# Kernel optimization log

Measured on AMD Instinct MI355X. Metric: run time of the kernel, lower is better.

## Reference

```python
import jax, jax.numpy as jnp
import numpy as np

L = 12; NH = 12; DH = 64; H = 768; FF = 3072; S = 1024; B = 4; V = 50265; WIN = 256  # one-sided window (attention_window=512)

def _ln(x, g, b, eps=1e-5):
    m = jnp.mean(x, axis=-1, keepdims=True)
    v = jnp.mean((x - m) ** 2, axis=-1, keepdims=True)
    return (x - m) * jax.lax.rsqrt(v + eps) * g + b

def _local_attn(q, k, v, mask, w):
    # q,k,v: [B,NH,S,DH]; mask: [B,S] ints (1=attend, 0=pad).
    # Sliding-window attention computed in query blocks of size w over key spans of 3w
    # (no global tokens: forward never passes a global_attention_mask).
    b, nh, s, dh = q.shape
    c = w; nb = s // c; span = 3 * c
    qb = q.reshape(b, nh, nb, c, dh)
    kp = jnp.pad(k, ((0, 0), (0, 0), (w, w), (0, 0)))
    vp = jnp.pad(v, ((0, 0), (0, 0), (w, w), (0, 0)))
    idx = jnp.arange(nb)[:, None] * c + jnp.arange(span)[None, :]  # [nb, span]
    kb = kp[:, :, idx]  # [B,NH,nb,span,DH]
    vb = vp[:, :, idx]
    scores = jnp.einsum('bhncd,bhnkd->bhnck', qb, kb) / np.float32(np.sqrt(dh))
    qi = jnp.arange(c)[:, None]; kj = jnp.arange(span)[None, :]
    band = (kj - qi >= 0) & (kj - qi <= 2 * w)  # |k_abs - q_abs| <= w
    mp = jnp.pad(mask, ((0, 0), (w, w)))  # zero pad also masks out-of-range keys
    mb = mp[:, idx] > 0  # [B, nb, span]
    ok = band[None, None, None, :, :] & mb[:, None, :, None, :]
    scores = jnp.where(ok, scores, jnp.float32(-1e9))
    probs = jax.nn.softmax(scores, axis=-1)
    out = jnp.einsum('bhnck,bhnkd->bhncd', probs, vb)
    return out.reshape(b, nh, s, dh)

def _forward(WE, PE, Eg, Eb, Wq, bq, Wk, bk, Wv, bv, Wo, bo, g1, beta1, W1, b1, W2, b2, g2, beta2, aw, Wc, bc, input_ids, attention_mask):
    b, s = input_ids.shape
    h = WE[input_ids] + PE[jnp.arange(s)]
    h = _ln(h, Eg, Eb)
    for l in range(L):
        q = (h @ Wq[l] + bq[l]).reshape(b, s, NH, DH).transpose(0, 2, 1, 3)
        k = (h @ Wk[l] + bk[l]).reshape(b, s, NH, DH).transpose(0, 2, 1, 3)
        v = (h @ Wv[l] + bv[l]).reshape(b, s, NH, DH).transpose(0, 2, 1, 3)
        a = _local_attn(q, k, v, attention_mask, WIN)
        a = a.transpose(0, 2, 1, 3).reshape(b, s, H) @ Wo[l] + bo[l]
        h = _ln(h + a, g1[l], beta1[l])
        f = jax.nn.gelu(h @ W1[l] + b1[l], approximate=False) @ W2[l] + b2[l]
        h = _ln(h + f, g2[l], beta2[l])
    # attention-pooling head: softmax over seq of h @ aw, weighted sum, linear classifier
    sc = h @ aw  # [B,S]
    probs = jax.nn.softmax(sc, axis=1)
    pooled = jnp.sum(h * probs[..., None], axis=1)  # [B,H]
    return pooled @ Wc + bc  # [B,1] (dropout is identity in eval)

def setup_inputs():
    key = jax.random.key(0)
    ks = jax.random.split(key, 16)
    n = lambda k, shape: 0.02 * jax.random.normal(k, shape, dtype=jnp.float32)
    return {
        'WE': n(ks[0], (V, H)), 'PE': n(ks[1], (S, H)),
        'Eg': jnp.ones((H,), jnp.float32), 'Eb': jnp.zeros((H,), jnp.float32),
        'Wq': n(ks[2], (L, H, H)), 'bq': jnp.zeros((L, H), jnp.float32),
        'Wk': n(ks[3], (L, H, H)), 'bk': jnp.zeros((L, H), jnp.float32),
        'Wv': n(ks[4], (L, H, H)), 'bv': jnp.zeros((L, H), jnp.float32),
        'Wo': n(ks[5], (L, H, H)), 'bo': jnp.zeros((L, H), jnp.float32),
        'g1': jnp.ones((L, H), jnp.float32), 'beta1': jnp.zeros((L, H), jnp.float32),
        'W1': n(ks[6], (L, H, FF)), 'b1': jnp.zeros((L, FF), jnp.float32),
        'W2': n(ks[7], (L, FF, H)), 'b2': jnp.zeros((L, H), jnp.float32),
        'g2': jnp.ones((L, H), jnp.float32), 'beta2': jnp.zeros((L, H), jnp.float32),
        'aw': jax.random.normal(ks[8], (H,), dtype=jnp.float32),
        'Wc': n(ks[9], (H, 1)), 'bc': jnp.zeros((1,), jnp.float32),
        'input_ids': jax.random.randint(ks[10], (B, S), 0, V, dtype=jnp.int32),
        'attention_mask': jnp.ones((B, S), jnp.int32),
    }

def reference(WE, PE, Eg, Eb, Wq, bq, Wk, bk, Wv, bv, Wo, bo, g1, beta1, W1, b1, W2, b2, g2, beta2, aw, Wc, bc, input_ids, attention_mask):
    return _forward(WE, PE, Eg, Eb, Wq, bq, Wk, bk, Wv, bv, Wo, bo, g1, beta1, W1, b1, W2, b2, g2, beta2, aw, Wc, bc, input_ids, attention_mask)
```

## Files before the change

kernel.cpp:

```cpp
#include <hip/hip_runtime.h>
#include <hip/hip_bf16.h>

#define LAYERS 12
#define NHEAD  12
#define DHEAD  64
#define HDIM   768
#define FFDIM  3072
#define SEQ    1024
#define BATCH  4
#define WINSZ  256
#define MTOK   (BATCH*SEQ)
#define PLANE  ((size_t)MTOK*HDIM)

typedef unsigned short u16;
typedef unsigned int   u32;

using f32x4  = __attribute__((ext_vector_type(4))) float;
using bf16x8 = __attribute__((ext_vector_type(8))) short;

__device__ __forceinline__ float bflo(u32 u){ union{u32 i;float f;}x; x.i = u << 16; return x.f; }
__device__ __forceinline__ float bfhi(u32 u){ union{u32 i;float f;}x; x.i = u & 0xffff0000u; return x.f; }
__device__ __forceinline__ u16 f2bf(float f){
    union{float f;u32 u;}x; x.f = f;
    u32 r = x.u + 0x7fffu + ((x.u >> 16) & 1u);
    return (u16)(r >> 16);
}
__device__ __forceinline__ void gload16(const u16* g, u16* l) {
    __builtin_amdgcn_global_load_lds(
        (const __attribute__((address_space(1))) u32*)g,
        (__attribute__((address_space(3))) u32*)l, 16, 0, 0);
}

__device__ __forceinline__ float wave_sum(float v) {
#pragma unroll
    for (int o = 32; o > 0; o >>= 1) v += __shfl_down(v, o, 64);
    return v;
}
__device__ __forceinline__ float wave_max(float v) {
#pragma unroll
    for (int o = 32; o > 0; o >>= 1) v = fmaxf(v, __shfl_down(v, o, 64));
    return v;
}
__device__ __forceinline__ float blk_sum256(float v, float* sm) {
    v = wave_sum(v);
    int lane = threadIdx.x & 63, w = threadIdx.x >> 6;
    __syncthreads();
    if (lane == 0) sm[w] = v;
    __syncthreads();
    return sm[0] + sm[1] + sm[2] + sm[3];
}
__device__ __forceinline__ float blk_sum1024(float v, float* sm) {
    v = wave_sum(v);
    int lane = threadIdx.x & 63, w = threadIdx.x >> 6;
    __syncthreads();
    if (lane == 0) sm[w] = v;
    __syncthreads();
    float r = 0.f;
#pragma unroll
    for (int i = 0; i < 16; i++) r += sm[i];
    return r;
}
__device__ __forceinline__ float blk_max1024(float v, float* sm) {
    v = wave_max(v);
    int lane = threadIdx.x & 63, w = threadIdx.x >> 6;
    __syncthreads();
    if (lane == 0) sm[w] = v;
    __syncthreads();
    float r = -1e30f;
#pragma unroll
    for (int i = 0; i < 16; i++) r = fmaxf(r, sm[i]);
    return r;
}

__global__ __launch_bounds__(256) void k_embed_ln(
    const float* __restrict__ WE, const float* __restrict__ PE,
    const float* __restrict__ g, const float* __restrict__ bta,
    const int* __restrict__ ids, float* __restrict__ h, u16* __restrict__ hb)
{
    __shared__ float sm[4];
    int tok = blockIdx.x;
    int s = tok & (SEQ - 1);
    int id = ids[tok];
    int tt = threadIdx.x;
    float4 x = make_float4(0.f, 0.f, 0.f, 0.f);
    if (tt < HDIM / 4) {
        float4 a = ((const float4*)(WE + (size_t)id * HDIM))[tt];
        float4 b = ((const float4*)(PE + (size_t)s * HDIM))[tt];
        x = make_float4(a.x + b.x, a.y + b.y, a.z + b.z, a.w + b.w);
    }
    float s1 = blk_sum256(x.x + x.y + x.z + x.w, sm);
    float s2 = blk_sum256(x.x*x.x + x.y*x.y + x.z*x.z + x.w*x.w, sm);
    float mean = s1 * (1.f / HDIM);
    float var  = s2 * (1.f / HDIM) - mean * mean;
    float inv  = rsqrtf(var + 1e-5f);
    if (tt < HDIM / 4) {
        float4 gg = ((const float4*)g)[tt];
        float4 bb = ((const float4*)bta)[tt];
        float4 o;
        o.x = (x.x - mean) * inv * gg.x + bb.x;
        o.y = (x.y - mean) * inv * gg.y + bb.y;
        o.z = (x.z - mean) * inv * gg.z + bb.z;
        o.w = (x.w - mean) * inv * gg.w + bb.w;
        ((float4*)(h + (size_t)tok * HDIM))[tt] = o;
        uint2 pk;
        pk.x = (u32)f2bf(o.x) | ((u32)f2bf(o.y) << 16);
        pk.y = (u32)f2bf(o.z) | ((u32)f2bf(o.w) << 16);
        ((uint2*)(hb + (size_t)tok * HDIM))[tt] = pk;
    }
}

__global__ __launch_bounds__(256) void k_addln(
    float* __restrict__ h, const float* __restrict__ t,
    const float* __restrict__ g, const float* __restrict__ bta, u16* __restrict__ hb)
{
    __shared__ float sm[4];
    int tok = blockIdx.x;
    int tt = threadIdx.x;
    float4 x = make_float4(0.f, 0.f, 0.f, 0.f);
    if (tt < HDIM / 4) {
        float4 a = ((const float4*)(h + (size_t)tok * HDIM))[tt];
        float4 b = ((const float4*)(t + (size_t)tok * HDIM))[tt];
        x = make_float4(a.x + b.x, a.y + b.y, a.z + b.z, a.w + b.w);
    }
    float s1 = blk_sum256(x.x + x.y + x.z + x.w, sm);
    float s2 = blk_sum256(x.x*x.x + x.y*x.y + x.z*x.z + x.w*x.w, sm);
    float mean = s1 * (1.f / HDIM);
    float var  = s2 * (1.f / HDIM) - mean * mean;
    float inv  = rsqrtf(var + 1e-5f);
    if (tt < HDIM / 4) {
        float4 gg = ((const float4*)g)[tt];
        float4 bb = ((const float4*)bta)[tt];
        float4 o;
        o.x = (x.x - mean) * inv * gg.x + bb.x;
        o.y = (x.y - mean) * inv * gg.y + bb.y;
        o.z = (x.z - mean) * inv * gg.z + bb.z;
        o.w = (x.w - mean) * inv * gg.w + bb.w;
        ((float4*)(h + (size_t)tok * HDIM))[tt] = o;
        uint2 pk;
        pk.x = (u32)f2bf(o.x) | ((u32)f2bf(o.y) << 16);
        pk.y = (u32)f2bf(o.z) | ((u32)f2bf(o.w) << 16);
        ((uint2*)(hb + (size_t)tok * HDIM))[tt] = pk;
    }
}

__global__ __launch_bounds__(256) void k_cvtT(
    const float* __restrict__ W, u16* __restrict__ dst, int K, int N,
    size_t ss, size_t ds)
{
    __shared__ float t[32][33];
    W   += (size_t)blockIdx.z * ss;
    dst += (size_t)blockIdx.z * ds;
    int n0 = blockIdx.x * 32, k0 = blockIdx.y * 32;
    int c = threadIdx.x & 31, r8 = threadIdx.x >> 5;
#pragma unroll
    for (int p = 0; p < 4; p++) {
        int k = r8 + p * 8;
        t[k][c] = W[(size_t)(k0 + k) * N + n0 + c];
    }
    __syncthreads();
#pragma unroll
    for (int p = 0; p < 2; p++) {
        int idx = threadIdx.x + p * 256;
        int n = idx >> 4, kp = idx & 15;
        float a = t[kp*2][n], b = t[kp*2+1][n];
        u32 pk = (u32)f2bf(a) | ((u32)f2bf(b) << 16);
        u32* d = (u32*)(dst + (size_t)(n0 + n) * K + k0);
        d[kp] = pk;
    }
}

template<int BM, int BN, int MODE>
__global__ __launch_bounds__(256) void k_gemm_mfma(
    const u16* __restrict__ A, const u16* __restrict__ BT,
    const float* __restrict__ b0, const float* __restrict__ b1, const float* __restrict__ b2,
    void* __restrict__ C, int K, int N)
{
    __shared__ u16 As[2 * BM * 32];
    __shared__ u16 Bs[2 * BN * 32];
    const int tid = threadIdx.x, lane = tid & 63, w = tid >> 6;
    const int bm = blockIdx.y * BM, bn = blockIdx.x * BN;
    constexpr int MT = BM / 32, NT = BN / 32;
    constexpr int AR = BM / 4, BR = BN / 4;
    constexpr int AI = AR / 16, BI = BR / 16;
    const int wm = (w & 1) * (BM / 2), wn = (w >> 1) * (BN / 2);

    f32x4 acc[MT][NT];
#pragma unroll
    for (int mi = 0; mi < MT; mi++)
#pragma unroll
        for (int ni = 0; ni < NT; ni++) acc[mi][ni] = (f32x4){0.f, 0.f, 0.f, 0.f};

    const u16* ag = A  + (size_t)(bm + w * AR + (lane >> 2)) * K + (lane & 3) * 8;
    const u16* bg = BT + (size_t)(bn + w * BR + (lane >> 2)) * K + (lane & 3) * 8;
    u16* al = As + w * AR * 32;
    u16* bl = Bs + w * BR * 32;
    const int fr = lane & 15, fq = (lane >> 4) * 8;

    for (int k0 = 0; k0 < K; k0 += 64) {
#pragma unroll
        for (int s = 0; s < 2; s++) {
#pragma unroll
            for (int i = 0; i < AI; i++)
                gload16(ag + (size_t)i * 16 * K + k0 + s * 32, al + s * BM * 32 + i * 512);
#pragma unroll
            for (int i = 0; i < BI; i++)
                gload16(bg + (size_t)i * 16 * K + k0 + s * 32, bl + s * BN * 32 + i * 512);
        }
        __syncthreads();
#pragma unroll
        for (int s = 0; s < 2; s++) {
            bf16x8 af[MT], bf[NT];
#pragma unroll
            for (int mi = 0; mi < MT; mi++)
                af[mi] = *(const bf16x8*)(As + s * BM * 32 + (wm + mi * 16 + fr) * 32 + fq);
#pragma unroll
            for (int ni = 0; ni < NT; ni++)
                bf[ni] = *(const bf16x8*)(Bs + s * BN * 32 + (wn + ni * 16 + fr) * 32 + fq);
#pragma unroll
            for (int mi = 0; mi < MT; mi++)
#pragma unroll
                for (int ni = 0; ni < NT; ni++)
                    acc[mi][ni] = __builtin_amdgcn_mfma_f32_16x16x32_bf16(af[mi], bf[ni], acc[mi][ni], 0, 0, 0);
        }
        __syncthreads();
    }

#pragma unroll
    for (int mi = 0; mi < MT; mi++) {
        int m_base = bm + wm + mi * 16 + (lane >> 4) * 4;
#pragma unroll
        for (int ni = 0; ni < NT; ni++) {
            int n_g = bn + wn + ni * 16 + (lane & 15);
            const float* bp = b0; int nn = n_g; int which = 0;
            if (MODE == 1) {
                if (n_g >= 1536)      { bp = b2; nn = n_g - 1536; which = 2; }
                else if (n_g >= 768)  { bp = b1; nn = n_g - 768;  which = 1; }
            }
            float bias = bp[nn];
#pragma unroll
            for (int r = 0; r < 4; r++) {
                int m_g = m_base + r;
                float val = acc[mi][ni][r] + bias;
                if (MODE == 0) {
                    ((float*)C)[(size_t)m_g * N + n_g] = val;
                } else if (MODE == 1) {
                    int bb = m_g >> 10, ss = m_g & 1023;
                    int hh = nn >> 6, dd = nn & 63;
                    ((u16*)C)[(size_t)which * PLANE + (((size_t)bb * NHEAD + hh) * SEQ + ss) * DHEAD + dd] = f2bf(val);
                } else {
                    val = 0.5f * val * (1.f + erff(val * 0.70710678118f));
                    ((u16*)C)[(size_t)m_g * N + n_g] = f2bf(val);
                }
            }
        }
    }
}

#define PADW 72
__global__ __launch_bounds__(256) void k_attn_mfma(
    const u16* __restrict__ qkv, const int* __restrict__ mask, u16* __restrict__ abuf)
{
    __shared__ u16 Qs[64 * PADW];
    __shared__ u16 Ks[64 * PADW];
    __shared__ u16 Vt[64 * PADW];
    __shared__ u16 Ps[64 * PADW];
    __shared__ int ms[64];
    const int tid = threadIdx.x, lane = tid & 63, w = tid >> 6;
    int blk = blockIdx.x;
    int qt = blk & 15;
    int hh = (blk >> 4) % NHEAD;
    int b  = blk / (16 * NHEAD);
    int q0 = qt * 64;

    const u16* qp = qkv + ((size_t)b * NHEAD + hh) * SEQ * DHEAD;
    const u16* kp = qp + PLANE;
    const u16* vp = qp + 2 * PLANE;

#pragma unroll
    for (int it = 0; it < 2; it++) {
        int idx = tid + it * 256;
        int r = idx >> 3, c8 = (idx & 7) * 8;
        uint4 u = *(const uint4*)(qp + (size_t)(q0 + r) * DHEAD + c8);
        *(uint4*)(Qs + r * PADW + c8) = u;
    }

    const int fr = lane & 15, g4 = (lane >> 4) * 4, fq = (lane >> 4) * 8;
    const int wq = w * 16;
    const int qpos = q0 + wq + g4;

    f32x4 o[4];
#pragma unroll
    for (int d = 0; d < 4; d++) o[d] = (f32x4){0.f, 0.f, 0.f, 0.f};
    float mr[4], ll[4];
#pragma unroll
    for (int r = 0; r < 4; r++) { mr[r] = -1e9f; ll[r] = 0.f; }

    __syncthreads();
    bf16x8 aq[2];
#pragma unroll
    for (int ks = 0; ks < 2; ks++)
        aq[ks] = *(const bf16x8*)(Qs + (wq + fr) * PADW + ks * 32 + fq);

    for (int ch = 0; ch < 9; ch++) {
        int kbase = q0 - 256 + ch * 64;
        __syncthreads();
#pragma unroll
        for (int it = 0; it < 2; it++) {
            int idx = tid + it * 256;
            int r = idx >> 3, c8 = (idx & 7) * 8;
            int kq = kbase + r;
            uint4 u = (kq >= 0 && kq < SEQ)
                ? *(const uint4*)(kp + (size_t)kq * DHEAD + c8)
                : make_uint4(0u, 0u, 0u, 0u);
            *(uint4*)(Ks + r * PADW + c8) = u;
        }
        {
            int r = tid >> 2, sg = (tid & 3) * 16;
            int kq = kbase + r;
            uint4 u0 = make_uint4(0u,0u,0u,0u), u1 = u0;
            if (kq >= 0 && kq < SEQ) {
                const uint4* vr = (const uint4*)(vp + (size_t)kq * DHEAD + sg);
                u0 = vr[0]; u1 = vr[1];
            }
            u32 ww[8] = {u0.x, u0.y, u0.z, u0.w, u1.x, u1.y, u1.z, u1.w};
#pragma unroll
            for (int j = 0; j < 8; j++) {
                Vt[(sg + 2*j    ) * PADW + r] = (u16)(ww[j] & 0xffffu);
                Vt[(sg + 2*j + 1) * PADW + r] = (u16)(ww[j] >> 16);
            }
        }
        if (tid < 64) {
            int kq = kbase + tid;
            ms[tid] = (kq >= 0 && kq < SEQ) ? mask[b * SEQ + kq] : 0;
        }
        __syncthreads();

        f32x4 s[4];
#pragma unroll
        for (int nt = 0; nt < 4; nt++) s[nt] = (f32x4){0.f, 0.f, 0.f, 0.f};
#pragma unroll
        for (int nt = 0; nt < 4; nt++)
#pragma unroll
            for (int ks = 0; ks < 2; ks++) {
                bf16x8 bk = *(const bf16x8*)(Ks + (nt*16 + fr) * PADW + ks*32 + fq);
                s[nt] = __builtin_amdgcn_mfma_f32_16x16x32_bf16(aq[ks], bk, s[nt], 0, 0, 0);
            }

        float mloc[4];
#pragma unroll
        for (int r = 0; r < 4; r++) mloc[r] = -1e9f;
#pragma unroll
        for (int nt = 0; nt < 4; nt++) {
            int kpos = kbase + nt*16 + fr;
            int msv = ms[nt*16 + fr];
#pragma unroll
            for (int r = 0; r < 4; r++) {
                int dq = kpos - (qpos + r);
                bool ok = (dq >= -WINSZ) && (dq <= WINSZ) && (msv != 0);
                float sv = ok ? s[nt][r] * 0.125f : -1e9f;
                s[nt][r] = sv;
                mloc[r] = fmaxf(mloc[r], sv);
            }
        }
#pragma unroll
        for (int mk = 1; mk < 16; mk <<= 1)
#pragma unroll
            for (int r = 0; r < 4; r++)
                mloc[r] = fmaxf(mloc[r], __shfl_xor(mloc[r], mk, 64));

        float sc4[4], psum[4];
#pragma unroll
        for (int r = 0; r < 4; r++) {
            float mn = fmaxf(mr[r], mloc[r]);
            sc4[r] = __expf(mr[r] - mn);
            mr[r] = mn;
            psum[r] = 0.f;
        }
#pragma unroll
        for (int nt = 0; nt < 4; nt++)
#pragma unroll
            for (int r = 0; r < 4; r++) {
                float p = (s[nt][r] > -1e8f) ? __expf(s[nt][r] - mr[r]) : 0.f;
                psum[r] += p;
                Ps[(wq + g4 + r) * PADW + nt*16 + fr] = f2bf(p);
            }
#pragma unroll
        for (int mk = 1; mk < 16; mk <<= 1)
#pragma unroll
            for (int r = 0; r < 4; r++)
                psum[r] += __shfl_xor(psum[r], mk, 64);

        f32x4 scv = (f32x4){sc4[0], sc4[1], sc4[2], sc4[3]};
#pragma unroll
        for (int r = 0; r < 4; r++) ll[r] = ll[r] * sc4[r] + psum[r];
#pragma unroll
        for (int d = 0; d < 4; d++) o[d] *= scv;

#pragma unroll
        for (int ks = 0; ks < 2; ks++) {
            bf16x8 ap = *(const bf16x8*)(Ps + (wq + fr) * PADW + ks*32 + fq);
#pragma unroll
            for (int d = 0; d < 4; d++) {
                bf16x8 bv8 = *(const bf16x8*)(Vt + (d*16 + fr) * PADW + ks*32 + fq);
                o[d] = __builtin_amdgcn_mfma_f32_16x16x32_bf16(ap, bv8, o[d], 0, 0, 0);
            }
        }
    }

#pragma unroll
    for (int r = 0; r < 4; r++) {
        float inv = 1.f / ll[r];
        u16* orow = abuf + ((size_t)(b * SEQ + q0 + wq + g4 + r)) * HDIM + hh * DHEAD;
#pragma unroll
        for (int d = 0; d < 4; d++)
            orow[d*16 + fr] = f2bf(o[d][r] * inv);
    }
}

__global__ __launch_bounds__(256) void k_pool_score(
    const float* __restrict__ h, const float* __restrict__ aw, float* __restrict__ sc)
{
    int tok = blockIdx.x * 4 + (threadIdx.x >> 6);
    int lane = threadIdx.x & 63;
    const float4* hr = (const float4*)(h + (size_t)tok * HDIM);
    const float4* ar = (const float4*)aw;
    float acc = 0.f;
#pragma unroll
    for (int i = 0; i < 3; i++) {
        int c = lane + i * 64;
        float4 x = hr[c], a = ar[c];
        acc += x.x*a.x + x.y*a.y + x.z*a.z + x.w*a.w;
    }
    acc = wave_sum(acc);
    if (lane == 0) sc[tok] = acc;
}

__global__ __launch_bounds__(1024) void k_pool_softmax(float* __restrict__ sc)
{
    __shared__ float red[16];
    int b = blockIdx.x;
    float v = sc[b * SEQ + threadIdx.x];
    float mx = blk_max1024(v, red);
    float e = __expf(v - mx);
    float tot = blk_sum1024(e, red);
    sc[b * SEQ + threadIdx.x] = e / tot;
}

__global__ __launch_bounds__(256) void k_pool_reduce(
    const float* __restrict__ h, const float* __restrict__ ps, float* __restrict__ partial)
{
    int b = blockIdx.x, j = blockIdx.y;
    int tid = threadIdx.x;
    const float* hb = h + ((size_t)b * SEQ + j * 64) * HDIM;
    const float* pp = ps + b * SEQ + j * 64;
    float a0 = 0.f, a1 = 0.f, a2 = 0.f;
    for (int s = 0; s < 64; s++) {
        float p = pp[s];
        const float* row = hb + (size_t)s * HDIM;
        a0 = fmaf(row[tid],       p, a0);
        a1 = fmaf(row[tid + 256], p, a1);
        a2 = fmaf(row[tid + 512], p, a2);
    }
    float* outp = partial + ((size_t)b * 16 + j) * HDIM;
    outp[tid] = a0; outp[tid + 256] = a1; outp[tid + 512] = a2;
}

__global__ __launch_bounds__(256) void k_pool_final(
    const float* __restrict__ partial, const float* __restrict__ Wc,
    const float* __restrict__ bc, float* __restrict__ out)
{
    __shared__ float sm[4];
    int b = blockIdx.x, tid = threadIdx.x;
    float acc = 0.f;
#pragma unroll
    for (int dd = 0; dd < 3; dd++) {
        int d = tid + dd * 256;
        float pd = 0.f;
#pragma unroll
        for (int j = 0; j < 16; j++)
            pd += partial[((size_t)b * 16 + j) * HDIM + d];
        acc = fmaf(pd, Wc[d], acc);
    }
    float total = blk_sum256(acc, sm);
    if (tid == 0) out[b] = total + bc[0];
}

extern "C" void kernel_launch(void* const* d_in, const int* in_sizes, int n_in,
                              void* d_out, int out_size, void* d_ws, size_t ws_size,
                              hipStream_t stream)
{
    const float* WE    = (const float*)d_in[0];
    const float* PE    = (const float*)d_in[1];
    const float* Eg    = (const float*)d_in[2];
    const float* Eb    = (const float*)d_in[3];
    const float* Wq    = (const float*)d_in[4];
    const float* bq    = (const float*)d_in[5];
    const float* Wk    = (const float*)d_in[6];
    const float* bk    = (const float*)d_in[7];
    const float* Wv    = (const float*)d_in[8];
    const float* bv    = (const float*)d_in[9];
    const float* Wo    = (const float*)d_in[10];
    const float* bo    = (const float*)d_in[11];
    const float* g1    = (const float*)d_in[12];
    const float* beta1 = (const float*)d_in[13];
    const float* W1    = (const float*)d_in[14];
    const float* b1    = (const float*)d_in[15];
    const float* W2    = (const float*)d_in[16];
    const float* b2    = (const float*)d_in[17];
    const float* g2    = (const float*)d_in[18];
    const float* beta2 = (const float*)d_in[19];
    const float* aw    = (const float*)d_in[20];
    const float* Wc    = (const float*)d_in[21];
    const float* bc    = (const float*)d_in[22];
    const int* ids     = (const int*)d_in[23];
    const int* msk     = (const int*)d_in[24];

    char* base = (char*)d_ws;
    float* h    = (float*)base;                               base += (size_t)MTOK * HDIM * 4;
    float* tbuf = (float*)base;                               base += (size_t)MTOK * HDIM * 4;
    u16*   hb   = (u16*)base;                                 base += (size_t)MTOK * HDIM * 2;
    u16*   X    = (u16*)base;                                 base += (size_t)MTOK * FFDIM * 2;
    u16*   qkv  = X;
    u16*   abuf = X + 3 * PLANE;
    u16*   mid  = X;

    const size_t sQKV = (size_t)2304 * HDIM;
    const size_t sWO  = (size_t)HDIM * HDIM;
    const size_t sW1  = (size_t)FFDIM * HDIM;
    const size_t sW2  = (size_t)HDIM * FFDIM;
    size_t fixed = (size_t)(base - (char*)d_ws);
    size_t all_bytes = fixed + (size_t)LAYERS * (sQKV + sWO + sW1 + sW2) * 2;
    bool wsall = ws_size >= all_bytes;
    int NL = wsall ? LAYERS : 1;
    u16* wqkvT = (u16*)base;
    u16* woT   = wqkvT + sQKV * NL;
    u16* w1T   = woT   + sWO  * NL;
    u16* w2T   = w1T   + sW1  * NL;

    k_embed_ln<<<MTOK, 256, 0, stream>>>(WE, PE, Eg, Eb, ids, h, hb);

    if (wsall) {
        k_cvtT<<<dim3(24, 24, LAYERS), 256, 0, stream>>>(Wq, wqkvT,                     HDIM, HDIM, (size_t)HDIM*HDIM, sQKV);
        k_cvtT<<<dim3(24, 24, LAYERS), 256, 0, stream>>>(Wk, wqkvT + (size_t)HDIM*HDIM, HDIM, HDIM, (size_t)HDIM*HDIM, sQKV);
        k_cvtT<<<dim3(24, 24, LAYERS), 256, 0, stream>>>(Wv, wqkvT + (size_t)2*HDIM*HDIM, HDIM, HDIM, (size_t)HDIM*HDIM, sQKV);
        k_cvtT<<<dim3(24, 24, LAYERS), 256, 0, stream>>>(Wo, woT, HDIM, HDIM, (size_t)HDIM*HDIM, sWO);
        k_cvtT<<<dim3(96, 24, LAYERS), 256, 0, stream>>>(W1, w1T, HDIM, FFDIM, (size_t)HDIM*FFDIM, sW1);
        k_cvtT<<<dim3(24, 96, LAYERS), 256, 0, stream>>>(W2, w2T, FFDIM, HDIM, (size_t)FFDIM*HDIM, sW2);
    }

    for (int l = 0; l < LAYERS; l++) {
        u16* wqkvT_l = wqkvT + (wsall ? (size_t)l * sQKV : 0);
        u16* woT_l   = woT   + (wsall ? (size_t)l * sWO  : 0);
        u16* w1T_l   = w1T   + (wsall ? (size_t)l * sW1  : 0);
        u16* w2T_l   = w2T   + (wsall ? (size_t)l * sW2  : 0);

        if (!wsall) {
            const float* Wql = Wq + (size_t)l * HDIM * HDIM;
            const float* Wkl = Wk + (size_t)l * HDIM * HDIM;
            const float* Wvl = Wv + (size_t)l * HDIM * HDIM;
            const float* Wol = Wo + (size_t)l * HDIM * HDIM;
            const float* W1l = W1 + (size_t)l * HDIM * FFDIM;
            const float* W2l = W2 + (size_t)l * FFDIM * HDIM;
            k_cvtT<<<dim3(24, 24), 256, 0, stream>>>(Wql, wqkvT_l,                      HDIM, HDIM, 0, 0);
            k_cvtT<<<dim3(24, 24), 256, 0, stream>>>(Wkl, wqkvT_l + (size_t)HDIM*HDIM,  HDIM, HDIM, 0, 0);
            k_cvtT<<<dim3(24, 24), 256, 0, stream>>>(Wvl, wqkvT_l + (size_t)2*HDIM*HDIM,HDIM, HDIM, 0, 0);
            k_cvtT<<<dim3(24, 24), 256, 0, stream>>>(Wol, woT_l, HDIM, HDIM, 0, 0);
            k_cvtT<<<dim3(96, 24), 256, 0, stream>>>(W1l, w1T_l, HDIM, FFDIM, 0, 0);
            k_cvtT<<<dim3(24, 96), 256, 0, stream>>>(W2l, w2T_l, FFDIM, HDIM, 0, 0);
        }

        k_gemm_mfma<128, 128, 1><<<dim3(2304/128, MTOK/128), 256, 0, stream>>>(
            hb, wqkvT_l, bq + l*HDIM, bk + l*HDIM, bv + l*HDIM, qkv, HDIM, 2304);
        k_attn_mfma<<<BATCH * NHEAD * (SEQ/64), 256, 0, stream>>>(qkv, msk, abuf);
        k_gemm_mfma<128, 64, 0><<<dim3(HDIM/64, MTOK/128), 256, 0, stream>>>(
            abuf, woT_l, bo + l*HDIM, nullptr, nullptr, tbuf, HDIM, HDIM);
        k_addln<<<MTOK, 256, 0, stream>>>(h, tbuf, g1 + l*HDIM, beta1 + l*HDIM, hb);
        k_gemm_mfma<128, 128, 2><<<dim3(FFDIM/128, MTOK/128), 256, 0, stream>>>(
            hb, w1T_l, b1 + l*FFDIM, nullptr, nullptr, mid, HDIM, FFDIM);
        k_gemm_mfma<128, 64, 0><<<dim3(HDIM/64, MTOK/128), 256, 0, stream>>>(
            mid, w2T_l, b2 + l*HDIM, nullptr, nullptr, tbuf, FFDIM, HDIM);
        k_addln<<<MTOK, 256, 0, stream>>>(h, tbuf, g2 + l*HDIM, beta2 + l*HDIM, hb);
    }

    float* ps      = tbuf;
    float* partial = tbuf + BATCH * SEQ;
    k_pool_score  <<<MTOK / 4, 256, 0, stream>>>(h, aw, ps);
    k_pool_softmax<<<BATCH, 1024, 0, stream>>>(ps);
    k_pool_reduce <<<dim3(BATCH, 16), 256, 0, stream>>>(h, ps, partial);
    k_pool_final  <<<BATCH, 256, 0, stream>>>(partial, Wc, bc, (float*)d_out);
}
```

Before: 2.776 ms.

## Fuse residual add into GEMM epilogue and widen K step to three sub-tiles

Adds a GEMM epilogue mode that adds the biased result straight into the fp32 residual stream `h`. This is used for the output-projection and FFN2 GEMMs, so the following layernorm kernel reads only `h` instead of `h` plus a temporary buffer. It also templates the number of 32-wide K sub-tiles loaded per barrier pair and raises it from 2 to 3 for all GEMMs. That means fewer `__syncthreads` per K loop, at the cost of more LDS per block, which can lower occupancy. The epilogue now does a read-modify-write on `h` instead of a plain store.

Result: slower. 3.146 ms (+13.3%).

```diff
diff --git a/kernel.cpp b/kernel.cpp
--- a/kernel.cpp
+++ b/kernel.cpp
@@ -109,8 +109,8 @@
     }
 }
 
-__global__ __launch_bounds__(256) void k_addln(
-    float* __restrict__ h, const float* __restrict__ t,
+__global__ __launch_bounds__(256) void k_ln(
+    float* __restrict__ h,
     const float* __restrict__ g, const float* __restrict__ bta, u16* __restrict__ hb)
 {
     __shared__ float sm[4];
@@ -118,9 +118,7 @@
     int tt = threadIdx.x;
     float4 x = make_float4(0.f, 0.f, 0.f, 0.f);
     if (tt < HDIM / 4) {
-        float4 a = ((const float4*)(h + (size_t)tok * HDIM))[tt];
-        float4 b = ((const float4*)(t + (size_t)tok * HDIM))[tt];
-        x = make_float4(a.x + b.x, a.y + b.y, a.z + b.z, a.w + b.w);
+        x = ((const float4*)(h + (size_t)tok * HDIM))[tt];
     }
     float s1 = blk_sum256(x.x + x.y + x.z + x.w, sm);
     float s2 = blk_sum256(x.x*x.x + x.y*x.y + x.z*x.z + x.w*x.w, sm);
@@ -169,14 +167,14 @@
     }
 }
 
-template<int BM, int BN, int MODE>
+template<int BM, int BN, int MODE, int NS>
 __global__ __launch_bounds__(256) void k_gemm_mfma(
     const u16* __restrict__ A, const u16* __restrict__ BT,
     const float* __restrict__ b0, const float* __restrict__ b1, const float* __restrict__ b2,
     void* __restrict__ C, int K, int N)
 {
-    __shared__ u16 As[2 * BM * 32];
-    __shared__ u16 Bs[2 * BN * 32];
+    __shared__ u16 As[NS * BM * 32];
+    __shared__ u16 Bs[NS * BN * 32];
     const int tid = threadIdx.x, lane = tid & 63, w = tid >> 6;
     const int bm = blockIdx.y * BM, bn = blockIdx.x * BN;
     constexpr int MT = BM / 32, NT = BN / 32;
@@ -196,9 +194,9 @@
     u16* bl = Bs + w * BR * 32;
     const int fr = lane & 15, fq = (lane >> 4) * 8;
 
-    for (int k0 = 0; k0 < K; k0 += 64) {
-#pragma unroll
-        for (int s = 0; s < 2; s++) {
+    for (int k0 = 0; k0 < K; k0 += 32 * NS) {
+#pragma unroll
+        for (int s = 0; s < NS; s++) {
 #pragma unroll
             for (int i = 0; i < AI; i++)
                 gload16(ag + (size_t)i * 16 * K + k0 + s * 32, al + s * BM * 32 + i * 512);
@@ -208,7 +206,7 @@
         }
         __syncthreads();
 #pragma unroll
-        for (int s = 0; s < 2; s++) {
+        for (int s = 0; s < NS; s++) {
             bf16x8 af[MT], bf[NT];
 #pragma unroll
             for (int mi = 0; mi < MT; mi++)
@@ -247,6 +245,9 @@
                     int bb = m_g >> 10, ss = m_g & 1023;
                     int hh = nn >> 6, dd = nn & 63;
                     ((u16*)C)[(size_t)which * PLANE + (((size_t)bb * NHEAD + hh) * SEQ + ss) * DHEAD + dd] = f2bf(val);
+                } else if (MODE == 3) {
+                    float* p = (float*)C + (size_t)m_g * N + n_g;
+                    *p += val;
                 } else {
                     val = 0.5f * val * (1.f + erff(val * 0.70710678118f));
                     ((u16*)C)[(size_t)m_g * N + n_g] = f2bf(val);
@@ -569,17 +570,17 @@
             k_cvtT<<<dim3(24, 96), 256, 0, stream>>>(W2l, w2T_l, FFDIM, HDIM, 0, 0);
         }
 
-        k_gemm_mfma<128, 128, 1><<<dim3(2304/128, MTOK/128), 256, 0, stream>>>(
+        k_gemm_mfma<128, 128, 1, 3><<<dim3(2304/128, MTOK/128), 256, 0, stream>>>(
             hb, wqkvT_l, bq + l*HDIM, bk + l*HDIM, bv + l*HDIM, qkv, HDIM, 2304);
         k_attn_mfma<<<BATCH * NHEAD * (SEQ/64), 256, 0, stream>>>(qkv, msk, abuf);
-        k_gemm_mfma<128, 64, 0><<<dim3(HDIM/64, MTOK/128), 256, 0, stream>>>(
-            abuf, woT_l, bo + l*HDIM, nullptr, nullptr, tbuf, HDIM, HDIM);
-        k_addln<<<MTOK, 256, 0, stream>>>(h, tbuf, g1 + l*HDIM, beta1 + l*HDIM, hb);
-        k_gemm_mfma<128, 128, 2><<<dim3(FFDIM/128, MTOK/128), 256, 0, stream>>>(
+        k_gemm_mfma<128, 64, 3, 3><<<dim3(HDIM/64, MTOK/128), 256, 0, stream>>>(
+            abuf, woT_l, bo + l*HDIM, nullptr, nullptr, h, HDIM, HDIM);
+        k_ln<<<MTOK, 256, 0, stream>>>(h, g1 + l*HDIM, beta1 + l*HDIM, hb);
+        k_gemm_mfma<128, 128, 2, 3><<<dim3(FFDIM/128, MTOK/128), 256, 0, stream>>>(
             hb, w1T_l, b1 + l*FFDIM, nullptr, nullptr, mid, HDIM, FFDIM);
-        k_gemm_mfma<128, 64, 0><<<dim3(HDIM/64, MTOK/128), 256, 0, stream>>>(
-            mid, w2T_l, b2 + l*HDIM, nullptr, nullptr, tbuf, FFDIM, HDIM);
-        k_addln<<<MTOK, 256, 0, stream>>>(h, tbuf, g2 + l*HDIM, beta2 + l*HDIM, hb);
+        k_gemm_mfma<128, 64, 3, 3><<<dim3(HDIM/64, MTOK/128), 256, 0, stream>>>(
+            mid, w2T_l, b2 + l*HDIM, nullptr, nullptr, h, FFDIM, HDIM);
+        k_ln<<<MTOK, 256, 0, stream>>>(h, g2 + l*HDIM, beta2 + l*HDIM, hb);
     }
 
     float* ps      = tbuf;
```
